# Kernel optimization log

Measured on AMD Instinct MI355X. Metric: run time of the kernel, lower is better.

Reference implementation:

```python
import jax, jax.numpy as jnp
import numpy as np

B, N, D = 1024, 32, 512  # graphs, node types (=nodes per graph), node_dim
EPS = 1e-5

def setup_inputs() -> dict:
    key = jax.random.key(0)
    ks = jax.random.split(key, 6)
    z = jax.random.normal(ks[0], (B, N, D), jnp.float32)
    # each graph contains every node type exactly once, in random order
    idx = jax.vmap(lambda k: jax.random.permutation(k, N))(jax.random.split(ks[1], B)).astype(jnp.int32)
    A = jax.random.normal(ks[2], (N, N), jnp.float32) / np.sqrt(N)
    W1 = jax.random.normal(ks[3], (N, D, 2 * D), jnp.float32) / np.sqrt(D)
    b1 = jnp.zeros((N, 2 * D), jnp.float32)
    W2 = jax.random.normal(ks[4], (N, 2 * D, D), jnp.float32) / np.sqrt(2 * D)
    b2 = jnp.zeros((N, D), jnp.float32)
    gamma = jnp.ones((D,), jnp.float32)
    beta = jnp.zeros((D,), jnp.float32)
    return dict(z=z, idx=idx, A=A, W1=W1, b1=b1, W2=W2, b2=b2, gamma=gamma, beta=beta)

def _layernorm(x, g, b):
    m = jnp.mean(x, axis=-1, keepdims=True)
    v = jnp.var(x, axis=-1, keepdims=True)
    return (x - m) * jax.lax.rsqrt(v + EPS) * g + b

def reference(z, idx, A, W1, b1, W2, b2, gamma, beta):
    # per-graph submatrix of global A: A_sub[b] = A[node_index, node_index]
    A_sub = A[idx[:, :, None], idx[:, None, :]]            # [B,K,K]
    # Az[b] = A_sub[b].T @ z[b]
    Az = jnp.einsum('bkj,bkd->bjd', A_sub, z)              # [B,K,D]
    Az = _layernorm(Az, gamma, beta)
    # route node of type t to expert t: inv[b,t] = position of type t in graph b
    inv = jnp.argsort(idx, axis=1)                         # [B,N]
    x = jnp.take_along_axis(Az, inv[:, :, None], axis=1)   # [B,N,D] type-ordered
    # per-type 2-layer MLP experts (Linear -> ELU -> Linear), dropout in eval mode
    h = jax.nn.elu(jnp.einsum('bnd,ndh->bnh', x, W1) + b1) # [B,N,2D]
    y = jnp.einsum('bnh,nhd->bnd', h, W2) + b2             # [B,N,D]
    # scatter back to node order: node j in graph b has type idx[b,j]
    mix = jnp.take_along_axis(y, idx[:, :, None].astype(jnp.int32), axis=1)
    return mix + Az
```

## Files before the change

kernel.cpp:

```cpp
#include <hip/hip_runtime.h>
#include <hip/hip_bf16.h>
#include <math.h>

#define B_  1024
#define N_  32
#define D_  512
#define EPS_ 1e-5f

typedef __attribute__((ext_vector_type(8))) short bf16x8;
typedef __attribute__((ext_vector_type(4))) float f32x4;
using bf16 = __hip_bfloat16;
typedef unsigned int u32;
typedef const u32 __attribute__((address_space(1)))* gp_t;
typedef u32 __attribute__((address_space(3)))* sp_t;

static __device__ __forceinline__ void gload16(const void* g, void* s) {
  __builtin_amdgcn_global_load_lds((gp_t)g, (sp_t)s, 16, 0, 0);
}
static __device__ __forceinline__ void bar() {
  asm volatile("s_barrier" ::: "memory");
}

static __device__ __forceinline__ unsigned short f2bf(float f) {
  union { float f; u32 u; } c; c.f = f;
  u32 r = c.u + 0x7fff + ((c.u >> 16) & 1);
  return (unsigned short)(r >> 16);
}
static __device__ __forceinline__ float bf2f(unsigned short h) {
  union { u32 u; float f; } c; c.u = ((u32)h) << 16;
  return c.f;
}

__global__ __launch_bounds__(256) void transpose_cast_kernel(
    const float* __restrict__ in, bf16* __restrict__ out, int R, int C) {
  __shared__ unsigned short tile[64][65];
  const size_t mat = (size_t)blockIdx.z * (size_t)R * (size_t)C;
  const float* inp = in + mat;
  bf16* outp = out + mat;
  const int c0 = blockIdx.x * 64, r0 = blockIdx.y * 64;
  const int tr = threadIdx.x >> 4;
  const int tc = (threadIdx.x & 15) * 4;
#pragma unroll
  for (int i = 0; i < 4; ++i) {
    const int r = tr + i * 16;
    float4 v = *(const float4*)&inp[(size_t)(r0 + r) * C + c0 + tc];
    tile[r][tc + 0] = f2bf(v.x);
    tile[r][tc + 1] = f2bf(v.y);
    tile[r][tc + 2] = f2bf(v.z);
    tile[r][tc + 3] = f2bf(v.w);
  }
  __syncthreads();
#pragma unroll
  for (int i = 0; i < 2; ++i) {
    const int chunk = i * 256 + threadIdx.x;
    const int c = chunk >> 3, r8 = (chunk & 7) * 8;
    union { bf16x8 v; unsigned short u[8]; } pk;
#pragma unroll
    for (int k = 0; k < 8; ++k) pk.u[k] = tile[r8 + k][c];
    *(bf16x8*)&outp[(size_t)(c0 + c) * R + r0 + r8] = pk.v;
  }
}

__global__ __launch_bounds__(256) void mix_ln_kernel(
    const float* __restrict__ z, const int* __restrict__ idx,
    const float* __restrict__ A, const float* __restrict__ gamma,
    const float* __restrict__ beta, bf16* __restrict__ x_ws,
    int* __restrict__ inv_ws) {
  __shared__ float As[32][32];
  __shared__ int   p[32];
  __shared__ float red1[4][32];
  __shared__ float red2[4][32];
  __shared__ float meanS[32];
  __shared__ float rstdS[32];

  const int b = blockIdx.x;
  const int t = threadIdx.x;
  const int lane = t & 63, wid = t >> 6;
  const int llo = lane & 15, lhi = lane >> 4;

  if (t < 32) {
    int v = idx[b * 32 + t];
    p[t] = v;
    inv_ws[b * 32 + v] = t;
  }
  __syncthreads();
#pragma unroll
  for (int i = 0; i < 4; ++i) {
    const int id = i * 256 + t;
    As[id >> 5][id & 31] = A[p[id >> 5] * 32 + (id & 31)];
  }
  __syncthreads();

  bf16x8 af[2];
#pragma unroll
  for (int nt = 0; nt < 2; ++nt) {
    union { bf16x8 v; unsigned short s[8]; } u;
#pragma unroll
    for (int j = 0; j < 8; ++j)
      u.s[j] = f2bf(As[lhi * 8 + j][nt * 16 + llo]);
    af[nt] = u.v;
  }

  const float* zb = z + (size_t)b * (N_ * D_) + (size_t)(lhi * 8) * D_ + llo;
  const f32x4 fz = {0.f, 0.f, 0.f, 0.f};
  f32x4 acc[2][8];
#pragma unroll
  for (int nt = 0; nt < 2; ++nt)
#pragma unroll
    for (int dt = 0; dt < 8; ++dt) acc[nt][dt] = fz;

#pragma unroll
  for (int h = 0; h < 2; ++h) {
    float zr[4][8];
#pragma unroll
    for (int dd = 0; dd < 4; ++dd)
#pragma unroll
      for (int j = 0; j < 8; ++j)
        zr[dd][j] = zb[j * D_ + ((wid * 8 + h * 4 + dd) * 16)];
#pragma unroll
    for (int dd = 0; dd < 4; ++dd) {
      const int dt = h * 4 + dd;
      union { bf16x8 v; unsigned short s[8]; } u;
#pragma unroll
      for (int j = 0; j < 8; ++j) u.s[j] = f2bf(zr[dd][j]);
      acc[0][dt] = __builtin_amdgcn_mfma_f32_16x16x32_bf16(af[0], u.v, acc[0][dt], 0, 0, 0);
      acc[1][dt] = __builtin_amdgcn_mfma_f32_16x16x32_bf16(af[1], u.v, acc[1][dt], 0, 0, 0);
    }
  }

  float s1[2][4], s2[2][4];
#pragma unroll
  for (int nt = 0; nt < 2; ++nt)
#pragma unroll
    for (int r = 0; r < 4; ++r) {
      float a = 0.f, q = 0.f;
#pragma unroll
      for (int dt = 0; dt < 8; ++dt) {
        float v = acc[nt][dt][r];
        a += v; q += v * v;
      }
#pragma unroll
      for (int mk = 1; mk < 16; mk <<= 1) {
        a += __shfl_xor(a, mk);
        q += __shfl_xor(q, mk);
      }
      s1[nt][r] = a; s2[nt][r] = q;
    }
  if (llo == 0) {
#pragma unroll
    for (int nt = 0; nt < 2; ++nt)
#pragma unroll
      for (int r = 0; r < 4; ++r) {
        const int n = nt * 16 + lhi * 4 + r;
        red1[wid][n] = s1[nt][r];
        red2[wid][n] = s2[nt][r];
      }
  }
  __syncthreads();
  if (t < 32) {
    float S1 = red1[0][t] + red1[1][t] + red1[2][t] + red1[3][t];
    float S2 = red2[0][t] + red2[1][t] + red2[2][t] + red2[3][t];
    float mean = S1 * (1.f / D_);
    float var  = S2 * (1.f / D_) - mean * mean;
    meanS[t] = mean;
    rstdS[t] = rsqrtf(var + EPS_);
  }
  __syncthreads();

  float gv[8], bev[8];
#pragma unroll
  for (int dt = 0; dt < 8; ++dt) {
    const int d = (wid * 8 + dt) * 16 + llo;
    gv[dt] = gamma[d]; bev[dt] = beta[d];
  }
#pragma unroll
  for (int nt = 0; nt < 2; ++nt)
#pragma unroll
    for (int r = 0; r < 4; ++r) {
      const int n = nt * 16 + lhi * 4 + r;
      const float mn = meanS[n], rs = rstdS[n];
      unsigned short* xrow = (unsigned short*)(x_ws + ((size_t)n * B_ + b) * D_);
#pragma unroll
      for (int dt = 0; dt < 8; ++dt) {
        const int d = (wid * 8 + dt) * 16 + llo;
        float v = (acc[nt][dt][r] - mn) * rs * gv[dt] + bev[dt];
        xrow[d] = f2bf(v);
      }
    }
}

#define STG_A(P, H, S) do {                                                   \
    const bf16* g_ = Ag + (size_t)((H) * 128) * KD + (S) * 64 + soff;         \
    gload16(g_, Alds + (P) * 32768 + (H) * 16384 + dof);                      \
    gload16(g_ + (size_t)64 * KD, Alds + (P) * 32768 + (H) * 16384 + 8192 + dof); \
  } while (0)
#define STG_B(P, H, S) do {                                                   \
    const bf16* g_ = Bg + (size_t)((H) * 128) * KD + (S) * 64 + soff;         \
    gload16(g_, Blds + (P) * 32768 + (H) * 16384 + dof);                      \
    gload16(g_ + (size_t)64 * KD, Blds + (P) * 32768 + (H) * 16384 + 8192 + dof); \
  } while (0)

#define RD_A(P, H) do {                                                       \
    const char* Ab_ = Alds + (P) * 32768 + (H) * 16384;                       \
    _Pragma("unroll")                                                         \
    for (int fi = 0; fi < 2; ++fi) {                                          \
      av[fi][0] = *(const bf16x8*)(Ab_ + raA + fi * 2048 + j16);              \
      av[fi][1] = *(const bf16x8*)(Ab_ + raA + fi * 2048 + (j16 ^ 64));       \
    }                                                                         \
  } while (0)
#define RD_B(P, H, BV) do {                                                   \
    const char* Bb_ = Blds + (P) * 32768 + (H) * 16384;                       \
    _Pragma("unroll")                                                         \
    for (int fj = 0; fj < 4; ++fj) {                                          \
      BV[fj][0] = *(const bf16x8*)(Bb_ + raB + fj * 2048 + j16);              \
      BV[fj][1] = *(const bf16x8*)(Bb_ + raB + fj * 2048 + (j16 ^ 64));       \
    }                                                                         \
  } while (0)

#define MMA16(QR, QC, BV) do {                                                \
    __builtin_amdgcn_s_setprio(1);                                            \
    _Pragma("unroll")                                                         \
    for (int fi = 0; fi < 2; ++fi)                                            \
      _Pragma("unroll")                                                       \
      for (int fj = 0; fj < 4; ++fj) {                                        \
        acc[QR][QC][fi][fj] = __builtin_amdgcn_mfma_f32_16x16x32_bf16(        \
            av[fi][0], BV[fj][0], acc[QR][QC][fi][fj], 0, 0, 0);              \
        acc[QR][QC][fi][fj] = __builtin_amdgcn_mfma_f32_16x16x32_bf16(        \
            av[fi][1], BV[fj][1], acc[QR][QC][fi][fj], 0, 0, 0);              \
      }                                                                       \
    __builtin_amdgcn_s_setprio(0);                                            \
  } while (0)

#define VMC4() asm volatile("s_waitcnt vmcnt(4)" ::: "memory")
#define VMC0() asm volatile("s_waitcnt vmcnt(0)" ::: "memory")

template <int KD, int NS>
static __device__ __forceinline__ void gemm8_core(
    const bf16* __restrict__ Ag, const bf16* __restrict__ Bg,
    char* __restrict__ Alds, char* __restrict__ Blds,
    f32x4 (&acc)[2][2][2][4], const int t) {
  const int lane = t & 63, wid = t >> 6;
  const int llo = lane & 15, lhi = lane >> 4;
  const int raA = ((wid & 3) * 32 + llo) * 128;
  const int raB = ((wid >> 2) * 64 + llo) * 128;
  const int j16 = (lhi ^ (llo & 7)) * 16;
  const int soff = (t >> 3) * KD + ((t ^ (t >> 3)) & 7) * 8;
  const int dof = wid * 1024;

  bf16x8 av[2][2], bv0[4][2], bv1[4][2];

  STG_A(0, 0, 0); STG_B(0, 0, 0); STG_A(0, 1, 0); STG_B(0, 1, 0);
  STG_A(1, 0, 1); STG_B(1, 0, 1);
  VMC4();
  bar();

#pragma unroll 1
  for (int it = 0; it < NS / 2; ++it) {
    const int s0 = 2 * it;
    RD_A(0, 0); RD_B(0, 0, bv0);
    if (s0 + 1 < NS) STG_A(1, 1, s0 + 1);
    bar(); MMA16(0, 0, bv0); bar();
    RD_B(0, 1, bv1);
    if (s0 + 1 < NS) STG_B(1, 1, s0 + 1);
    bar(); MMA16(0, 1, bv1); bar();
    RD_A(0, 1);
    if (s0 + 2 < NS) STG_A(0, 0, s0 + 2);
    bar(); MMA16(1, 1, bv1); bar();
    if (s0 + 2 < NS) STG_B(0, 0, s0 + 2);
    bar(); MMA16(1, 0, bv0);
    if (s0 + 2 < NS) { VMC4(); } else { VMC0(); }
    bar();
    const int s1 = s0 + 1;
    RD_A(1, 0); RD_B(1, 0, bv0);
    if (s1 + 1 < NS) STG_A(0, 1, s1 + 1);
    bar(); MMA16(0, 0, bv0); bar();
    RD_B(1, 1, bv1);
    if (s1 + 1 < NS) STG_B(0, 1, s1 + 1);
    bar(); MMA16(0, 1, bv1); bar();
    RD_A(1, 1);
    if (s1 + 2 < NS) STG_A(1, 0, s1 + 2);
    bar(); MMA16(1, 1, bv1); bar();
    if (s1 + 2 < NS) STG_B(1, 0, s1 + 2);
    bar(); MMA16(1, 0, bv0);
    if (s1 + 2 < NS) { VMC4(); } else { VMC0(); }
    bar();
  }
}

__global__ __launch_bounds__(512, 2) void gemm1_kernel(
    const bf16* __restrict__ X,
    const bf16* __restrict__ W1t,
    const float* __restrict__ b1,
    bf16* __restrict__ Hout) {
  extern __shared__ char lds[];
  char* Alds = lds;
  char* Blds = lds + 65536;

  const int bid = blockIdx.x;
  const int swz = (bid & 7) * 64 + (bid >> 3);
  const int m  = swz >> 4;
  const int r_ = swz & 15;
  const int hb = r_ >> 2, bb = r_ & 3;

  const int t = threadIdx.x;
  const int lane = t & 63, wid = t >> 6;
  const int llo = lane & 15, lhi = lane >> 4;

  const bf16* Ag = W1t + (size_t)m * (1024 * 512) + (size_t)(hb * 256) * 512;
  const bf16* Bg = X   + (size_t)m * (1024 * 512) + (size_t)(bb * 256) * 512;

  const f32x4 fzero = {0.f, 0.f, 0.f, 0.f};
  f32x4 acc[2][2][2][4];
#pragma unroll
  for (int a = 0; a < 2; ++a)
#pragma unroll
    for (int b = 0; b < 2; ++b)
#pragma unroll
      for (int c = 0; c < 2; ++c)
#pragma unroll
        for (int d = 0; d < 4; ++d) acc[a][b][c][d] = fzero;

  gemm8_core<512, 8>(Ag, Bg, Alds, Blds, acc, t);

  const float* b1m = b1 + m * 1024 + hb * 256;
#pragma unroll
  for (int qr = 0; qr < 2; ++qr)
#pragma unroll
    for (int fi = 0; fi < 2; ++fi) {
      const int h_loc = qr * 128 + (wid & 3) * 32 + fi * 16 + lhi * 4;
      const float4 bi = *(const float4*)&b1m[h_loc];
#pragma unroll
      for (int qc = 0; qc < 2; ++qc)
#pragma unroll
        for (int fj = 0; fj < 4; ++fj) {
          const int b_loc = qc * 128 + (wid >> 2) * 64 + fj * 16 + llo;
          float v0 = acc[qr][qc][fi][fj][0] + bi.x;
          float v1 = acc[qr][qc][fi][fj][1] + bi.y;
          float v2 = acc[qr][qc][fi][fj][2] + bi.z;
          float v3 = acc[qr][qc][fi][fj][3] + bi.w;
          v0 = v0 > 0.f ? v0 : __expf(v0) - 1.0f;
          v1 = v1 > 0.f ? v1 : __expf(v1) - 1.0f;
          v2 = v2 > 0.f ? v2 : __expf(v2) - 1.0f;
          v3 = v3 > 0.f ? v3 : __expf(v3) - 1.0f;
          ushort4 pk;
          pk.x = f2bf(v0); pk.y = f2bf(v1); pk.z = f2bf(v2); pk.w = f2bf(v3);
          const int byte = (b_loc * 512 + h_loc * 2) ^ ((b_loc & 7) << 4);
          *(ushort4*)(lds + byte) = pk;
        }
    }
  __syncthreads();
  bf16* Hm = Hout + (size_t)m * (1024 * 1024);
  const int b0 = bb * 256, h0 = hb * 256;
#pragma unroll
  for (int r = 0; r < 16; ++r) {
    const int chunk = r * 512 + t;
    const int bl = chunk >> 5, hc = chunk & 31;
    const int byte = (bl * 512 + hc * 16) ^ ((bl & 7) << 4);
    bf16x8 v = *(const bf16x8*)(lds + byte);
    *(bf16x8*)&Hm[(size_t)(b0 + bl) * 1024 + h0 + hc * 8] = v;
  }
}

__global__ __launch_bounds__(512, 2) void gemm2_kernel(
    const bf16* __restrict__ Hin,
    const bf16* __restrict__ W2t,
    const float* __restrict__ b2,
    const bf16* __restrict__ Xb,
    const int* __restrict__ inv,
    float* __restrict__ out) {
  extern __shared__ char lds[];
  char* Alds = lds;
  char* Blds = lds + 65536;

  const int bid = blockIdx.x;
  const int swz = (bid & 7) * 32 + (bid >> 3);
  const int m  = swz >> 3;
  const int r_ = swz & 7;
  const int db_ = r_ >> 2, bb = r_ & 3;

  const int t = threadIdx.x;
  const int lane = t & 63, wid = t >> 6;
  const int llo = lane & 15, lhi = lane >> 4;

  const bf16* Ag = W2t + (size_t)m * (512 * 1024) + (size_t)(db_ * 256) * 1024;
  const bf16* Bg = Hin + (size_t)m * (1024 * 1024) + (size_t)(bb * 256) * 1024;

  const f32x4 fzero = {0.f, 0.f, 0.f, 0.f};
  f32x4 acc[2][2][2][4];
#pragma unroll
  for (int a = 0; a < 2; ++a)
#pragma unroll
    for (int b = 0; b < 2; ++b)
#pragma unroll
      for (int c = 0; c < 2; ++c)
#pragma unroll
        for (int d = 0; d < 4; ++d) acc[a][b][c][d] = fzero;

  gemm8_core<1024, 16>(Ag, Bg, Alds, Blds, acc, t);

  const float* b2m = b2 + m * 512;
  const bf16* Xm = Xb + (size_t)m * (1024 * 512);
#pragma unroll
  for (int qc = 0; qc < 2; ++qc)
#pragma unroll
    for (int fj = 0; fj < 4; ++fj) {
      const int b_ = bb * 256 + qc * 128 + (wid >> 2) * 64 + fj * 16 + llo;
      const int n_out = inv[b_ * 32 + m];
      float* orow = out + ((size_t)b_ * 32 + n_out) * 512;
      const bf16* xrow = Xm + (size_t)b_ * 512;
#pragma unroll
      for (int qr = 0; qr < 2; ++qr)
#pragma unroll
        for (int fi = 0; fi < 2; ++fi) {
          const int d0 = db_ * 256 + qr * 128 + (wid & 3) * 32 + fi * 16 + lhi * 4;
          const float4 bi = *(const float4*)&b2m[d0];
          const ushort4 xr = *(const ushort4*)&xrow[d0];
          float4 v;
          v.x = acc[qr][qc][fi][fj][0] + bi.x + bf2f(xr.x);
          v.y = acc[qr][qc][fi][fj][1] + bi.y + bf2f(xr.y);
          v.z = acc[qr][qc][fi][fj][2] + bi.z + bf2f(xr.z);
          v.w = acc[qr][qc][fi][fj][3] + bi.w + bf2f(xr.w);
          *(float4*)&orow[d0] = v;
        }
    }
}

extern "C" void kernel_launch(void* const* d_in, const int* in_sizes, int n_in,
                              void* d_out, int out_size, void* d_ws, size_t ws_size,
                              hipStream_t stream) {
  const float* z     = (const float*)d_in[0];
  const int*   idx   = (const int*)d_in[1];
  const float* A     = (const float*)d_in[2];
  const float* W1    = (const float*)d_in[3];
  const float* b1    = (const float*)d_in[4];
  const float* W2    = (const float*)d_in[5];
  const float* b2    = (const float*)d_in[6];
  const float* gamma = (const float*)d_in[7];
  const float* beta  = (const float*)d_in[8];
  float* out = (float*)d_out;
  char* ws = (char*)d_ws;

  const size_t OFF_X   = 0;
  const size_t OFF_H   = 33554432;
  const size_t OFF_W1T = 100663296;
  const size_t OFF_W2T = 134217728;
  const size_t OFF_INV = 167772160;
  const size_t NEED    = 167903232;
  if (ws_size < NEED) return;

  bf16* Xb  = (bf16*)(ws + OFF_X);
  bf16* Hb  = (bf16*)(ws + OFF_H);
  bf16* W1t = (bf16*)(ws + OFF_W1T);
  bf16* W2t = (bf16*)(ws + OFF_W2T);
  int*  inv = (int*)(ws + OFF_INV);

  hipFuncSetAttribute((const void*)gemm1_kernel,
                      hipFuncAttributeMaxDynamicSharedMemorySize, 131072);
  hipFuncSetAttribute((const void*)gemm2_kernel,
                      hipFuncAttributeMaxDynamicSharedMemorySize, 131072);

  transpose_cast_kernel<<<dim3(16, 8, 32), 256, 0, stream>>>(W1, W1t, 512, 1024);
  transpose_cast_kernel<<<dim3(8, 16, 32), 256, 0, stream>>>(W2, W2t, 1024, 512);

  mix_ln_kernel<<<dim3(B_), 256, 0, stream>>>(z, idx, A, gamma, beta, Xb, inv);

  gemm1_kernel<<<dim3(512), 512, 131072, stream>>>(Xb, W1t, b1, Hb);
  gemm2_kernel<<<dim3(256), 512, 131072, stream>>>(Hb, W2t, b2, Xb, inv, out);
}
```

Baseline: 168.5 us.

## Shrink GEMM tiles to 256x128 with 32-wide K steps for higher occupancy

Both expert GEMMs move from 256x256 output tiles with 64-wide K stages to 256x128 tiles with 32-wide K stages, which cuts LDS from 128KB to 48KB per block. Launch bounds rise from 2 to 4 blocks per CU and the grids double. The goal is better latency hiding and fuller use of the 256 CUs, since the old grids of 512 and 256 blocks underfilled the machine. In exchange, per-tile operand reuse drops, there are twice as many barriers per K element, and the epilogue staging in gemm1 is split into two passes.

```diff
diff --git a/kernel.cpp b/kernel.cpp
--- a/kernel.cpp
+++ b/kernel.cpp
@@ -189,179 +189,151 @@
     }
 }
 
-#define STG_A(P, H, S) do {                                                   \
-    const bf16* g_ = Ag + (size_t)((H) * 128) * KD + (S) * 64 + soff;         \
-    gload16(g_, Alds + (P) * 32768 + (H) * 16384 + dof);                      \
-    gload16(g_ + (size_t)64 * KD, Alds + (P) * 32768 + (H) * 16384 + 8192 + dof); \
+#define STGA(P, H, S)                                                         \
+  gload16(Ag + (size_t)((H) * 128) * KD + (S) * 32 + soff,                    \
+          lds + (P) * 16384 + (H) * 8192 + dof)
+#define STGB(P, S)                                                            \
+  gload16(Bg + (size_t)(S) * 32 + soff, lds + 32768 + (P) * 8192 + dof)
+
+#define RDA(P, H, AV) do {                                                    \
+    const char* base_ = lds + (P) * 16384 + (H) * 8192;                       \
+    AV[0] = *(const bf16x8*)(base_ + raA + j16);                              \
+    AV[1] = *(const bf16x8*)(base_ + raA + 1024 + j16);                       \
   } while (0)
-#define STG_B(P, H, S) do {                                                   \
-    const bf16* g_ = Bg + (size_t)((H) * 128) * KD + (S) * 64 + soff;         \
-    gload16(g_, Blds + (P) * 32768 + (H) * 16384 + dof);                      \
-    gload16(g_ + (size_t)64 * KD, Blds + (P) * 32768 + (H) * 16384 + 8192 + dof); \
+#define RDB(P) do {                                                           \
+    const char* base_ = lds + 32768 + (P) * 8192;                             \
+    _Pragma("unroll")                                                         \
+    for (int fj = 0; fj < 4; ++fj)                                            \
+      bv[fj] = *(const bf16x8*)(base_ + raB + fj * 1024 + j16);               \
   } while (0)
 
-#define RD_A(P, H) do {                                                       \
-    const char* Ab_ = Alds + (P) * 32768 + (H) * 16384;                       \
-    _Pragma("unroll")                                                         \
-    for (int fi = 0; fi < 2; ++fi) {                                          \
-      av[fi][0] = *(const bf16x8*)(Ab_ + raA + fi * 2048 + j16);              \
-      av[fi][1] = *(const bf16x8*)(Ab_ + raA + fi * 2048 + (j16 ^ 64));       \
-    }                                                                         \
-  } while (0)
-#define RD_B(P, H, BV) do {                                                   \
-    const char* Bb_ = Blds + (P) * 32768 + (H) * 16384;                       \
-    _Pragma("unroll")                                                         \
-    for (int fj = 0; fj < 4; ++fj) {                                          \
-      BV[fj][0] = *(const bf16x8*)(Bb_ + raB + fj * 2048 + j16);              \
-      BV[fj][1] = *(const bf16x8*)(Bb_ + raB + fj * 2048 + (j16 ^ 64));       \
-    }                                                                         \
-  } while (0)
-
-#define MMA16(QR, QC, BV) do {                                                \
+#define MMA8(QR, AV) do {                                                     \
     __builtin_amdgcn_s_setprio(1);                                            \
     _Pragma("unroll")                                                         \
     for (int fi = 0; fi < 2; ++fi)                                            \
       _Pragma("unroll")                                                       \
-      for (int fj = 0; fj < 4; ++fj) {                                        \
-        acc[QR][QC][fi][fj] = __builtin_amdgcn_mfma_f32_16x16x32_bf16(        \
-            av[fi][0], BV[fj][0], acc[QR][QC][fi][fj], 0, 0, 0);              \
-        acc[QR][QC][fi][fj] = __builtin_amdgcn_mfma_f32_16x16x32_bf16(        \
-            av[fi][1], BV[fj][1], acc[QR][QC][fi][fj], 0, 0, 0);              \
-      }                                                                       \
+      for (int fj = 0; fj < 4; ++fj)                                          \
+        acc[QR][fi][fj] = __builtin_amdgcn_mfma_f32_16x16x32_bf16(            \
+            AV[fi], bv[fj], acc[QR][fi][fj], 0, 0, 0);                        \
     __builtin_amdgcn_s_setprio(0);                                            \
   } while (0)
 
-#define VMC4() asm volatile("s_waitcnt vmcnt(4)" ::: "memory")
+#define VMC2() asm volatile("s_waitcnt vmcnt(2)" ::: "memory")
 #define VMC0() asm volatile("s_waitcnt vmcnt(0)" ::: "memory")
 
 template <int KD, int NS>
-static __device__ __forceinline__ void gemm8_core(
+static __device__ __forceinline__ void gemm_core(
     const bf16* __restrict__ Ag, const bf16* __restrict__ Bg,
-    char* __restrict__ Alds, char* __restrict__ Blds,
-    f32x4 (&acc)[2][2][2][4], const int t) {
+    char* __restrict__ lds, f32x4 (&acc)[2][2][4], const int t) {
   const int lane = t & 63, wid = t >> 6;
   const int llo = lane & 15, lhi = lane >> 4;
-  const int raA = ((wid & 3) * 32 + llo) * 128;
-  const int raB = ((wid >> 2) * 64 + llo) * 128;
-  const int j16 = (lhi ^ (llo & 7)) * 16;
-  const int soff = (t >> 3) * KD + ((t ^ (t >> 3)) & 7) * 8;
+  const int raA = ((wid & 3) * 32 + llo) * 64;
+  const int raB = ((wid >> 2) * 64 + llo) * 64;
+  const int j16 = ((lhi ^ (llo & 3)) & 3) * 16;
+  const int soff = (t >> 2) * KD + ((t ^ (t >> 2)) & 3) * 8;
   const int dof = wid * 1024;
 
-  bf16x8 av[2][2], bv0[4][2], bv1[4][2];
-
-  STG_A(0, 0, 0); STG_B(0, 0, 0); STG_A(0, 1, 0); STG_B(0, 1, 0);
-  STG_A(1, 0, 1); STG_B(1, 0, 1);
-  VMC4();
+  bf16x8 av0[2], av1[2], bv[4];
+
+  STGA(0, 0, 0); STGA(0, 1, 0); STGB(0, 0);
+  STGA(1, 0, 1); STGB(1, 1);
+  VMC2();
   bar();
 
 #pragma unroll 1
   for (int it = 0; it < NS / 2; ++it) {
     const int s0 = 2 * it;
-    RD_A(0, 0); RD_B(0, 0, bv0);
-    if (s0 + 1 < NS) STG_A(1, 1, s0 + 1);
-    bar(); MMA16(0, 0, bv0); bar();
-    RD_B(0, 1, bv1);
-    if (s0 + 1 < NS) STG_B(1, 1, s0 + 1);
-    bar(); MMA16(0, 1, bv1); bar();
-    RD_A(0, 1);
-    if (s0 + 2 < NS) STG_A(0, 0, s0 + 2);
-    bar(); MMA16(1, 1, bv1); bar();
-    if (s0 + 2 < NS) STG_B(0, 0, s0 + 2);
-    bar(); MMA16(1, 0, bv0);
-    if (s0 + 2 < NS) { VMC4(); } else { VMC0(); }
+    RDA(0, 0, av0); RDB(0);
+    if (s0 + 1 < NS) STGA(1, 1, s0 + 1);
+    bar(); MMA8(0, av0); bar();
+    RDA(0, 1, av1);
+    if (s0 + 2 < NS) { STGA(0, 0, s0 + 2); STGB(0, s0 + 2); }
+    bar(); MMA8(1, av1);
+    if (s0 + 2 < NS) { VMC2(); } else { VMC0(); }
     bar();
     const int s1 = s0 + 1;
-    RD_A(1, 0); RD_B(1, 0, bv0);
-    if (s1 + 1 < NS) STG_A(0, 1, s1 + 1);
-    bar(); MMA16(0, 0, bv0); bar();
-    RD_B(1, 1, bv1);
-    if (s1 + 1 < NS) STG_B(0, 1, s1 + 1);
-    bar(); MMA16(0, 1, bv1); bar();
-    RD_A(1, 1);
-    if (s1 + 2 < NS) STG_A(1, 0, s1 + 2);
-    bar(); MMA16(1, 1, bv1); bar();
-    if (s1 + 2 < NS) STG_B(1, 0, s1 + 2);
-    bar(); MMA16(1, 0, bv0);
-    if (s1 + 2 < NS) { VMC4(); } else { VMC0(); }
+    RDA(1, 0, av0); RDB(1);
+    if (s1 + 1 < NS) STGA(0, 1, s1 + 1);
+    bar(); MMA8(0, av0); bar();
+    RDA(1, 1, av1);
+    if (s1 + 2 < NS) { STGA(1, 0, s1 + 2); STGB(1, s1 + 2); }
+    bar(); MMA8(1, av1);
+    if (s1 + 2 < NS) { VMC2(); } else { VMC0(); }
     bar();
   }
 }
 
-__global__ __launch_bounds__(512, 2) void gemm1_kernel(
+__global__ __launch_bounds__(512, 4) void gemm1_kernel(
     const bf16* __restrict__ X,
     const bf16* __restrict__ W1t,
     const float* __restrict__ b1,
     bf16* __restrict__ Hout) {
   extern __shared__ char lds[];
-  char* Alds = lds;
-  char* Blds = lds + 65536;
 
   const int bid = blockIdx.x;
-  const int swz = (bid & 7) * 64 + (bid >> 3);
-  const int m  = swz >> 4;
-  const int r_ = swz & 15;
-  const int hb = r_ >> 2, bb = r_ & 3;
+  const int swz = (bid & 7) * 128 + (bid >> 3);
+  const int m  = swz >> 5;
+  const int r_ = swz & 31;
+  const int hb = r_ >> 3, bb = r_ & 7;
 
   const int t = threadIdx.x;
   const int lane = t & 63, wid = t >> 6;
   const int llo = lane & 15, lhi = lane >> 4;
 
   const bf16* Ag = W1t + (size_t)m * (1024 * 512) + (size_t)(hb * 256) * 512;
-  const bf16* Bg = X   + (size_t)m * (1024 * 512) + (size_t)(bb * 256) * 512;
+  const bf16* Bg = X   + (size_t)m * (1024 * 512) + (size_t)(bb * 128) * 512;
 
   const f32x4 fzero = {0.f, 0.f, 0.f, 0.f};
-  f32x4 acc[2][2][2][4];
+  f32x4 acc[2][2][4];
 #pragma unroll
   for (int a = 0; a < 2; ++a)
 #pragma unroll
-    for (int b = 0; b < 2; ++b)
-#pragma unroll
-      for (int c = 0; c < 2; ++c)
-#pragma unroll
-        for (int d = 0; d < 4; ++d) acc[a][b][c][d] = fzero;
-
-  gemm8_core<512, 8>(Ag, Bg, Alds, Blds, acc, t);
-
-  const float* b1m = b1 + m * 1024 + hb * 256;
-#pragma unroll
-  for (int qr = 0; qr < 2; ++qr)
+    for (int c = 0; c < 2; ++c)
+#pragma unroll
+      for (int d = 0; d < 4; ++d) acc[a][c][d] = fzero;
+
+  gemm_core<512, 16>(Ag, Bg, lds, acc, t);
+
+  bf16* Hm = Hout + (size_t)m * (1024 * 1024);
+  const int b0 = bb * 128, h0 = hb * 256;
+#pragma unroll 1
+  for (int qr = 0; qr < 2; ++qr) {
+    __syncthreads();
+    const float* b1m = b1 + m * 1024 + h0 + qr * 128;
 #pragma unroll
     for (int fi = 0; fi < 2; ++fi) {
-      const int h_loc = qr * 128 + (wid & 3) * 32 + fi * 16 + lhi * 4;
+      const int h_loc = (wid & 3) * 32 + fi * 16 + lhi * 4;
       const float4 bi = *(const float4*)&b1m[h_loc];
 #pragma unroll
-      for (int qc = 0; qc < 2; ++qc)
-#pragma unroll
-        for (int fj = 0; fj < 4; ++fj) {
-          const int b_loc = qc * 128 + (wid >> 2) * 64 + fj * 16 + llo;
-          float v0 = acc[qr][qc][fi][fj][0] + bi.x;
-          float v1 = acc[qr][qc][fi][fj][1] + bi.y;
-          float v2 = acc[qr][qc][fi][fj][2] + bi.z;
-          float v3 = acc[qr][qc][fi][fj][3] + bi.w;
-          v0 = v0 > 0.f ? v0 : __expf(v0) - 1.0f;
-          v1 = v1 > 0.f ? v1 : __expf(v1) - 1.0f;
-          v2 = v2 > 0.f ? v2 : __expf(v2) - 1.0f;
-          v3 = v3 > 0.f ? v3 : __expf(v3) - 1.0f;
-          ushort4 pk;
-          pk.x = f2bf(v0); pk.y = f2bf(v1); pk.z = f2bf(v2); pk.w = f2bf(v3);
-          const int byte = (b_loc * 512 + h_loc * 2) ^ ((b_loc & 7) << 4);
-          *(ushort4*)(lds + byte) = pk;
-        }
+      for (int fj = 0; fj < 4; ++fj) {
+        const int b_loc = (wid >> 2) * 64 + fj * 16 + llo;
+        float v0 = acc[qr][fi][fj][0] + bi.x;
+        float v1 = acc[qr][fi][fj][1] + bi.y;
+        float v2 = acc[qr][fi][fj][2] + bi.z;
+        float v3 = acc[qr][fi][fj][3] + bi.w;
+        v0 = v0 > 0.f ? v0 : __expf(v0) - 1.0f;
+        v1 = v1 > 0.f ? v1 : __expf(v1) - 1.0f;
+        v2 = v2 > 0.f ? v2 : __expf(v2) - 1.0f;
+        v3 = v3 > 0.f ? v3 : __expf(v3) - 1.0f;
+        ushort4 pk;
+        pk.x = f2bf(v0); pk.y = f2bf(v1); pk.z = f2bf(v2); pk.w = f2bf(v3);
+        const int byte = (b_loc * 256 + h_loc * 2) ^ ((b_loc & 7) << 4);
+        *(ushort4*)(lds + byte) = pk;
+      }
     }
-  __syncthreads();
-  bf16* Hm = Hout + (size_t)m * (1024 * 1024);
-  const int b0 = bb * 256, h0 = hb * 256;
-#pragma unroll
-  for (int r = 0; r < 16; ++r) {
-    const int chunk = r * 512 + t;
-    const int bl = chunk >> 5, hc = chunk & 31;
-    const int byte = (bl * 512 + hc * 16) ^ ((bl & 7) << 4);
-    bf16x8 v = *(const bf16x8*)(lds + byte);
-    *(bf16x8*)&Hm[(size_t)(b0 + bl) * 1024 + h0 + hc * 8] = v;
-  }
-}
-
-__global__ __launch_bounds__(512, 2) void gemm2_kernel(
+    __syncthreads();
+#pragma unroll
+    for (int i = 0; i < 4; ++i) {
+      const int c = i * 512 + t;
+      const int bl = c >> 4, hc = c & 15;
+      const int byte = (bl * 256 + hc * 16) ^ ((bl & 7) << 4);
+      bf16x8 v = *(const bf16x8*)(lds + byte);
+      *(bf16x8*)&Hm[(size_t)(b0 + bl) * 1024 + h0 + qr * 128 + hc * 8] = v;
+    }
+  }
+}
+
+__global__ __launch_bounds__(512, 4) void gemm2_kernel(
     const bf16* __restrict__ Hin,
     const bf16* __restrict__ W2t,
     const float* __restrict__ b2,
@@ -369,60 +341,54 @@
     const int* __restrict__ inv,
     float* __restrict__ out) {
   extern __shared__ char lds[];
-  char* Alds = lds;
-  char* Blds = lds + 65536;
 
   const int bid = blockIdx.x;
-  const int swz = (bid & 7) * 32 + (bid >> 3);
-  const int m  = swz >> 3;
-  const int r_ = swz & 7;
-  const int db_ = r_ >> 2, bb = r_ & 3;
+  const int swz = (bid & 7) * 64 + (bid >> 3);
+  const int m  = swz >> 4;
+  const int r_ = swz & 15;
+  const int db_ = r_ >> 3, bb = r_ & 7;
 
   const int t = threadIdx.x;
   const int lane = t & 63, wid = t >> 6;
   const int llo = lane & 15, lhi = lane >> 4;
 
   const bf16* Ag = W2t + (size_t)m * (512 * 1024) + (size_t)(db_ * 256) * 1024;
-  const bf16* Bg = Hin + (size_t)m * (1024 * 1024) + (size_t)(bb * 256) * 1024;
+  const bf16* Bg = Hin + (size_t)m * (1024 * 1024) + (size_t)(bb * 128) * 1024;
 
   const f32x4 fzero = {0.f, 0.f, 0.f, 0.f};
-  f32x4 acc[2][2][2][4];
+  f32x4 acc[2][2][4];
 #pragma unroll
   for (int a = 0; a < 2; ++a)
 #pragma unroll
-    for (int b = 0; b < 2; ++b)
-#pragma unroll
-      for (int c = 0; c < 2; ++c)
-#pragma unroll
-        for (int d = 0; d < 4; ++d) acc[a][b][c][d] = fzero;
-
-  gemm8_core<1024, 16>(Ag, Bg, Alds, Blds, acc, t);
+    for (int c = 0; c < 2; ++c)
+#pragma unroll
+      for (int d = 0; d < 4; ++d) acc[a][c][d] = fzero;
+
+  gemm_core<1024, 32>(Ag, Bg, lds, acc, t);
 
   const float* b2m = b2 + m * 512;
   const bf16* Xm = Xb + (size_t)m * (1024 * 512);
 #pragma unroll
-  for (int qc = 0; qc < 2; ++qc)
-#pragma unroll
-    for (int fj = 0; fj < 4; ++fj) {
-      const int b_ = bb * 256 + qc * 128 + (wid >> 2) * 64 + fj * 16 + llo;
-      const int n_out = inv[b_ * 32 + m];
-      float* orow = out + ((size_t)b_ * 32 + n_out) * 512;
-      const bf16* xrow = Xm + (size_t)b_ * 512;
-#pragma unroll
-      for (int qr = 0; qr < 2; ++qr)
-#pragma unroll
-        for (int fi = 0; fi < 2; ++fi) {
-          const int d0 = db_ * 256 + qr * 128 + (wid & 3) * 32 + fi * 16 + lhi * 4;
-          const float4 bi = *(const float4*)&b2m[d0];
-          const ushort4 xr = *(const ushort4*)&xrow[d0];
-          float4 v;
-          v.x = acc[qr][qc][fi][fj][0] + bi.x + bf2f(xr.x);
-          v.y = acc[qr][qc][fi][fj][1] + bi.y + bf2f(xr.y);
-          v.z = acc[qr][qc][fi][fj][2] + bi.z + bf2f(xr.z);
-          v.w = acc[qr][qc][fi][fj][3] + bi.w + bf2f(xr.w);
-          *(float4*)&orow[d0] = v;
-        }
-    }
+  for (int fj = 0; fj < 4; ++fj) {
+    const int b_ = bb * 128 + (wid >> 2) * 64 + fj * 16 + llo;
+    const int n_out = inv[b_ * 32 + m];
+    float* orow = out + ((size_t)b_ * 32 + n_out) * 512;
+    const bf16* xrow = Xm + (size_t)b_ * 512;
+#pragma unroll
+    for (int qr = 0; qr < 2; ++qr)
+#pragma unroll
+      for (int fi = 0; fi < 2; ++fi) {
+        const int d0 = db_ * 256 + qr * 128 + (wid & 3) * 32 + fi * 16 + lhi * 4;
+        const float4 bi = *(const float4*)&b2m[d0];
+        const ushort4 xr = *(const ushort4*)&xrow[d0];
+        float4 v;
+        v.x = acc[qr][fi][fj][0] + bi.x + bf2f(xr.x);
+        v.y = acc[qr][fi][fj][1] + bi.y + bf2f(xr.y);
+        v.z = acc[qr][fi][fj][2] + bi.z + bf2f(xr.z);
+        v.w = acc[qr][fi][fj][3] + bi.w + bf2f(xr.w);
+        *(float4*)&orow[d0] = v;
+      }
+  }
 }
 
 extern "C" void kernel_launch(void* const* d_in, const int* in_sizes, int n_in,
@@ -455,15 +421,15 @@
   int*  inv = (int*)(ws + OFF_INV);
 
   hipFuncSetAttribute((const void*)gemm1_kernel,
-                      hipFuncAttributeMaxDynamicSharedMemorySize, 131072);
+                      hipFuncAttributeMaxDynamicSharedMemorySize, 49152);
   hipFuncSetAttribute((const void*)gemm2_kernel,
-                      hipFuncAttributeMaxDynamicSharedMemorySize, 131072);
+                      hipFuncAttributeMaxDynamicSharedMemorySize, 49152);
 
   transpose_cast_kernel<<<dim3(16, 8, 32), 256, 0, stream>>>(W1, W1t, 512, 1024);
   transpose_cast_kernel<<<dim3(8, 16, 32), 256, 0, stream>>>(W2, W2t, 1024, 512);
 
   mix_ln_kernel<<<dim3(B_), 256, 0, stream>>>(z, idx, A, gamma, beta, Xb, inv);
 
-  gemm1_kernel<<<dim3(512), 512, 131072, stream>>>(Xb, W1t, b1, Hb);
-  gemm2_kernel<<<dim3(256), 512, 131072, stream>>>(Hb, W2t, b2, Xb, inv, out);
-}
+  gemm1_kernel<<<dim3(1024), 512, 49152, stream>>>(Xb, W1t, b1, Hb);
+  gemm2_kernel<<<dim3(512), 512, 49152, stream>>>(Hb, W2t, b2, Xb, inv, out);
+}
```

Result: slower. 269.5 us (+59.9%).
